# Optimization experiments

Hardware: AMD Instinct MI355X
Metric: run time of the kernel (lower is better)

The kernel has to match this reference:

```python
import jax, jax.numpy as jnp
import numpy as np

N_HEAD = 16

def setup_inputs() -> dict:
    key = jax.random.key(0)
    ks = jax.random.split(key, 9)
    B, S, D = 8, 1024, 1024
    s = 0.02
    return {
        "x":    jax.random.normal(ks[0], (B, S, D), dtype=jnp.float32),
        "mask": jax.random.normal(ks[1], (S, S), dtype=jnp.float32),
        "Wq":   jax.random.normal(ks[2], (D, D), dtype=jnp.float32) * s,
        "bq":   jax.random.normal(ks[3], (D,), dtype=jnp.float32) * s,
        "Wk":   jax.random.normal(ks[4], (D, D), dtype=jnp.float32) * s,
        "Wv":   jax.random.normal(ks[5], (D, D), dtype=jnp.float32) * s,
        "bv":   jax.random.normal(ks[6], (D,), dtype=jnp.float32) * s,
        "Wo":   jax.random.normal(ks[7], (D, D), dtype=jnp.float32) * s,
        "bo":   jax.random.normal(ks[8], (D,), dtype=jnp.float32) * s,
    }

def reference(x, mask, Wq, bq, Wk, Wv, bv, Wo, bo):
    B, S, D = x.shape
    H = N_HEAD
    dh = D // H
    scale = dh ** (-0.25)
    # projections (F.linear: x @ W.T + b); key has no bias
    q = x @ Wq.T + bq
    k = x @ Wk.T
    v = x @ Wv.T + bv
    # [B,S,D] -> [B,H,S,dh]; scale applied to both q and k
    q = q.reshape(B, S, H, dh).transpose(0, 2, 1, 3) * scale
    k = k.reshape(B, S, H, dh).transpose(0, 2, 1, 3) * scale
    v = v.reshape(B, S, H, dh).transpose(0, 2, 1, 3)
    qk = jnp.einsum("bhqd,bhkd->bhqk", q, k) + mask  # [B,H,S,S]
    w = jax.nn.softmax(qk.astype(jnp.float32), axis=-1).astype(q.dtype)
    wv = jnp.einsum("bhqk,bhkd->bhqd", w, v)
    wv = wv.transpose(0, 2, 1, 3).reshape(B, S, D)
    out = wv @ Wo.T + bo
    return out, qk
```

## Files before the change

### kernel.cpp

```cpp
#include <hip/hip_runtime.h>


typedef unsigned short u16;
typedef unsigned int   u32;
typedef __attribute__((ext_vector_type(8)))  __bf16 bf16x8;
typedef __attribute__((ext_vector_type(4)))  float  f32x4;
typedef __attribute__((ext_vector_type(16))) float  f32x16;

__device__ __forceinline__ u16 f2bf(float f) {
  u32 u = __float_as_uint(f);
  u += 0x7FFFu + ((u >> 16) & 1u);
  return (u16)(u >> 16);
}
__device__ __forceinline__ float bf2f(u16 v) {
  return __uint_as_float(((u32)v) << 16);
}
__device__ __forceinline__ u32 pk2(float a, float b) {
  return (u32)f2bf(a) | ((u32)f2bf(b) << 16);
}
__device__ __forceinline__ f32x4 mfma16(bf16x8 a, bf16x8 b, f32x4 c) {
  return __builtin_amdgcn_mfma_f32_16x16x32_bf16(a, b, c, 0, 0, 0);
}
__device__ __forceinline__ f32x16 mfma32(bf16x8 a, bf16x8 b, f32x16 c) {
  return __builtin_amdgcn_mfma_f32_32x32x16_bf16(a, b, c, 0, 0, 0);
}
typedef __attribute__((address_space(3))) u32 lds_u32;
typedef const __attribute__((address_space(1))) u32 glb_u32;
__device__ __forceinline__ void gld_lds16(u16* lds, const u16* g) {
  __builtin_amdgcn_global_load_lds((glb_u32*)g, (lds_u32*)lds, 16, 0, 0);
}
__device__ __forceinline__ bf16x8 ld_bf8(const u16* p) {
  return *(const bf16x8*)p;
}

__global__ __launch_bounds__(256) void cvt_all(
    const float* __restrict__ x,
    const float* __restrict__ Wq, const float* __restrict__ Wk,
    const float* __restrict__ Wv, const float* __restrict__ Wo,
    u16* __restrict__ xb, u16* __restrict__ Wqb, u16* __restrict__ Wkb,
    u16* __restrict__ Wvb, u16* __restrict__ Wob) {
  const size_t i = (size_t)(blockIdx.x * 256 + threadIdx.x) * 8;
  const float* s; u16* d; size_t off;
  if      (i <  8388608) { s = x;  d = xb;  off = i; }
  else if (i <  9437184) { s = Wq; d = Wqb; off = i -  8388608; }
  else if (i < 10485760) { s = Wk; d = Wkb; off = i -  9437184; }
  else if (i < 11534336) { s = Wv; d = Wvb; off = i - 10485760; }
  else                   { s = Wo; d = Wob; off = i - 11534336; }
  const float4* sp = (const float4*)(s + off);
  float4 a = sp[0], b = sp[1];
  u16 r[8];
  r[0] = f2bf(a.x); r[1] = f2bf(a.y); r[2] = f2bf(a.z); r[3] = f2bf(a.w);
  r[4] = f2bf(b.x); r[5] = f2bf(b.y); r[6] = f2bf(b.z); r[7] = f2bf(b.w);
  *(uint4*)(d + off) = *(const uint4*)r;
}

__global__ __launch_bounds__(256) void trans_mask(
    const float* __restrict__ m, u16* __restrict__ mt) {
  __shared__ u16 L[32][33];
  const int x = threadIdx.x & 31, y4 = threadIdx.x >> 5;
  const int r0 = blockIdx.y * 32, c0 = blockIdx.x * 32;
#pragma unroll
  for (int j = 0; j < 4; ++j) {
    const int r = y4 * 4 + j;
    L[x][r] = f2bf(m[(r0 + r) * 1024 + c0 + x]);
  }
  __syncthreads();
#pragma unroll
  for (int j = 0; j < 4; ++j) {
    const int rr = y4 * 4 + j;
    mt[(c0 + rr) * 1024 + r0 + x] = L[rr][x];
  }
}

__global__ __launch_bounds__(256) void mask_pack(
    const u16* __restrict__ mt, u16* __restrict__ mp) {
  const int id = blockIdx.x * 256 + threadIdx.x;
  const int q  = id & 1023;
  const int hi = (id >> 10) & 1;
  const int c  = id >> 11;
  u16 r0[8], r1[8];
#pragma unroll
  for (int r = 0; r < 8; ++r)
    r0[r] = mt[(32 * c + (r & 3) + 8 * (r >> 2) + 4 * hi) * 1024 + q];
#pragma unroll
  for (int r = 8; r < 16; ++r)
    r1[r - 8] = mt[(32 * c + (r & 3) + 8 * (r >> 2) + 4 * hi) * 1024 + q];
  u16* dst = mp + ((size_t)((c * 2 + hi) * 1024 + q)) * 16;
  *(uint4*)dst       = *(const uint4*)r0;
  *(uint4*)(dst + 8) = *(const uint4*)r1;
}

__global__ __launch_bounds__(256) void proj_gemm(
    const u16* __restrict__ xb,
    const u16* __restrict__ Wqb, const u16* __restrict__ Wkb,
    const u16* __restrict__ Wvb,
    const float* __restrict__ bq, const float* __restrict__ bv,
    u16* __restrict__ Qt2, u16* __restrict__ Kt2, u16* __restrict__ V2) {
  __shared__ u16 As[2][128][32];
  __shared__ u16 Bs[2][128][32];
  const int tid  = threadIdx.x;
  const int lane = tid & 63;
  const int wid  = tid >> 6;
  const int c15  = lane & 15, c4 = lane >> 4;
  const int m0   = blockIdx.x * 128;
  const int nv0  = blockIdx.y * 128;
  const int region = nv0 >> 10;
  const int nl0  = nv0 & 1023;
  const u16* Wsrc = (region == 0) ? Wqb : (region == 1) ? Wkb : Wvb;
  const int wrow = wid >> 1, wcol = wid & 1;
  const int srow = lane >> 2, scol = (lane & 3) * 8;

  const u16* aptr = xb   + (m0  + srow) * 1024 + scol;
  const u16* bptr = Wsrc + (nl0 + srow) * 1024 + scol;

  f32x4 acc[4][4] = {};

#pragma unroll
  for (int j = 0; j < 2; ++j) {
    const int r = 64 * j + 16 * wid;
    gld_lds16(&As[0][r][0], aptr + r * 1024);
    gld_lds16(&Bs[0][r][0], bptr + r * 1024);
  }
  __syncthreads();

  int cur = 0;
  for (int k0 = 0; k0 < 1024; k0 += 32) {
    if (k0 + 32 < 1024) {
      const int nxt = cur ^ 1;
#pragma unroll
      for (int j = 0; j < 2; ++j) {
        const int r = 64 * j + 16 * wid;
        gld_lds16(&As[nxt][r][0], aptr + r * 1024 + k0 + 32);
        gld_lds16(&Bs[nxt][r][0], bptr + r * 1024 + k0 + 32);
      }
    }
    bf16x8 af[4], bfr[4];
#pragma unroll
    for (int a = 0; a < 4; ++a) af[a]  = ld_bf8(&As[cur][64 * wrow + 16 * a + c15][8 * c4]);
#pragma unroll
    for (int b = 0; b < 4; ++b) bfr[b] = ld_bf8(&Bs[cur][64 * wcol + 16 * b + c15][8 * c4]);
#pragma unroll
    for (int a = 0; a < 4; ++a)
#pragma unroll
      for (int b = 0; b < 4; ++b)
        acc[a][b] = mfma16(af[a], bfr[b], acc[a][b]);
    __syncthreads();
    cur ^= 1;
  }

  const float kSc = 0.35355339059327373f;
#pragma unroll
  for (int a = 0; a < 4; ++a) {
    const int mg = m0 + 64 * wrow + 16 * a + 4 * c4;
    const int bb = mg >> 10;
    const int sl = mg & 1023;
#pragma unroll
    for (int b = 0; b < 4; ++b) {
      const int nl = 64 * wcol + 16 * b + c15;
      const int nv = nv0 + nl;
      if (region == 0) {
        const int n = nv;
        const float bias = bq[n];
        u16* qp = Qt2 + (((bb * 16 + (n >> 6)) * 8 + ((n >> 3) & 7)) * 1024 + sl) * 8 + (n & 7);
#pragma unroll
        for (int j = 0; j < 4; ++j)
          qp[j * 8] = f2bf((acc[a][b][j] + bias) * kSc);
      } else if (region == 1) {
        const int n = nv - 1024;
        u16* kp = Kt2 + (((bb * 16 + (n >> 6)) * 8 + ((n >> 3) & 7)) * 1024 + sl) * 8 + (n & 7);
#pragma unroll
        for (int j = 0; j < 4; ++j)
          kp[j * 8] = f2bf(acc[a][b][j] * kSc);
      } else {
        const int n = nv - 2048;
        const float bias = bv[n];
        u16* vp = V2 + (((bb * 16 + (n >> 6)) * 128 + (sl >> 3)) * 64 + (n & 63)) * 8 + (sl & 7);
        u16 p[4];
#pragma unroll
        for (int j = 0; j < 4; ++j) p[j] = f2bf(acc[a][b][j] + bias);
        *(uint2*)vp = *(const uint2*)p;
      }
    }
  }
}

__global__ __launch_bounds__(256) void attn_v4(
    const u16* __restrict__ Qt2, const u16* __restrict__ Kt2,
    const u16* __restrict__ V2, const u16* __restrict__ maskP,
    float* __restrict__ qk, u16* __restrict__ WV) {
  __shared__ float Tb[4][32 * 34];
  __shared__ float invl[4][32];
  __shared__ float factw[4][32];
  const int tid  = threadIdx.x;
  const int lane = tid & 63;
  const int w    = tid >> 6;
  const int r31  = lane & 31, hi = lane >> 5;
  const int h = blockIdx.y, b = blockIdx.z;
  const int bh  = b * 16 + h;
  const int q0  = blockIdx.x * 128 + w * 32;
  const int bs0 = b * 1024;

  const u16* qbase = Qt2 + (size_t)bh * 65536;
  const u16* kbase = Kt2 + (size_t)bh * 65536;
  const u16* vbase = V2  + (size_t)bh * 65536;
  float* Tw = Tb[w];
  float* qkbase = qk + ((size_t)bh * 1024 + q0) * 1024;

  bf16x8 qf[4];
#pragma unroll
  for (int kk = 0; kk < 4; ++kk)
    qf[kk] = ld_bf8(qbase + ((2 * kk + hi) * 1024 + q0 + r31) * 8);

  const u16* mrow = maskP + ((size_t)(hi * 1024 + q0 + r31)) * 16;

  float m_run = -3e38f, l = 0.f;
  f32x16 oa0 = {}, oa1 = {};

  bf16x8 kc[4];
#pragma unroll
  for (int kk = 0; kk < 4; ++kk)
    kc[kk] = ld_bf8(kbase + ((2 * kk + hi) * 1024 + r31) * 8);
  bf16x8 mc0 = ld_bf8(mrow);
  bf16x8 mc1 = ld_bf8(mrow + 8);

  for (int c = 0; c < 32; ++c) {
    bf16x8 vf[4];
#pragma unroll
    for (int kk = 0; kk < 2; ++kk) {
      const int sb = 4 * c + 2 * kk + hi;
      vf[2 * kk]     = ld_bf8(vbase + (sb * 64 + r31) * 8);
      vf[2 * kk + 1] = ld_bf8(vbase + (sb * 64 + 32 + r31) * 8);
    }
    const int cn = (c < 31) ? c + 1 : 31;
    bf16x8 kn[4];
#pragma unroll
    for (int kk = 0; kk < 4; ++kk)
      kn[kk] = ld_bf8(kbase + ((2 * kk + hi) * 1024 + 32 * cn + r31) * 8);
    bf16x8 mn0 = ld_bf8(mrow + (size_t)cn * 32768);
    bf16x8 mn1 = ld_bf8(mrow + (size_t)cn * 32768 + 8);

    f32x16 acc = {};
#pragma unroll
    for (int kk = 0; kk < 4; ++kk)
      acc = mfma32(kc[kk], qf[kk], acc);

    float v[16];
    float mloc = -3e38f;
    const u16* mcu0 = (const u16*)&mc0;
    const u16* mcu1 = (const u16*)&mc1;
#pragma unroll
    for (int r = 0; r < 16; ++r) {
      v[r] = acc[r] + bf2f(r < 8 ? mcu0[r] : mcu1[r - 8]);
      mloc = fmaxf(mloc, v[r]);
    }
    mloc = fmaxf(mloc, __shfl_xor(mloc, 32));

#pragma unroll
    for (int g = 0; g < 4; ++g) {
      float2 w0; w0.x = v[4 * g];     w0.y = v[4 * g + 1];
      float2 w1; w1.x = v[4 * g + 2]; w1.y = v[4 * g + 3];
      *(float2*)&Tw[r31 * 34 + 8 * g + 4 * hi]     = w0;
      *(float2*)&Tw[r31 * 34 + 8 * g + 4 * hi + 2] = w1;
    }

    if (!__all(mloc <= m_run + 8.f)) {
      const float m_new = fmaxf(m_run, mloc);
      const float f = __expf(m_run - m_new);
      l *= f;
      if (hi == 0) factw[w][r31] = f;
      asm volatile("s_waitcnt lgkmcnt(0)" ::: "memory");
#pragma unroll
      for (int r = 0; r < 16; ++r) {
        const float fr_ = factw[w][(r & 3) + 8 * (r >> 2) + 4 * hi];
        oa0[r] *= fr_;
        oa1[r] *= fr_;
      }
      m_run = m_new;
    }

#pragma unroll
    for (int qi = 0; qi < 4; ++qi) {
      const int qq = 8 * qi + (lane >> 3);
      const int jj = (lane & 7) * 4;
      float2 u0 = *(const float2*)&Tw[qq * 34 + jj];
      float2 u1 = *(const float2*)&Tw[qq * 34 + jj + 2];
      f32x4 o; o[0] = u0.x; o[1] = u0.y; o[2] = u1.x; o[3] = u1.y;
      *(f32x4*)&qkbase[qq * 1024 + 32 * c + jj] = o;
    }

#pragma unroll
    for (int r = 0; r < 16; ++r) {
      v[r] = __expf(v[r] - m_run);
      l += v[r];
    }

#pragma unroll
    for (int kk = 0; kk < 2; ++kk) {
      const float* pp = v + 8 * kk;
      const u32 a0 = pk2(pp[0], pp[1]), a1 = pk2(pp[2], pp[3]);
      const u32 b0 = pk2(pp[4], pp[5]), b1 = pk2(pp[6], pp[7]);
      const u32 s0 = hi ? a0 : b0, s1 = hi ? a1 : b1;
      const u32 t0 = __shfl_xor(s0, 32), t1 = __shfl_xor(s1, 32);
      union { u32 u[4]; bf16x8 v; } fr;
      fr.u[0] = hi ? t0 : a0;  fr.u[1] = hi ? t1 : a1;
      fr.u[2] = hi ? b0 : t0;  fr.u[3] = hi ? b1 : t1;
      oa0 = mfma32(fr.v, vf[2 * kk],     oa0);
      oa1 = mfma32(fr.v, vf[2 * kk + 1], oa1);
    }

#pragma unroll
    for (int kk = 0; kk < 4; ++kk) kc[kk] = kn[kk];
    mc0 = mn0; mc1 = mn1;
  }

  l += __shfl_xor(l, 32);
  if (hi == 0) invl[w][r31] = 1.0f / l;
  asm volatile("s_waitcnt lgkmcnt(0)" ::: "memory");
#pragma unroll
  for (int r = 0; r < 16; ++r) {
    const int q = (r & 3) + 8 * (r >> 2) + 4 * hi;
    const float iv = invl[w][q];
    u16* wp = WV + (size_t)(bs0 + q0 + q) * 1024 + h * 64;
    wp[r31]      = f2bf(oa0[r] * iv);
    wp[32 + r31] = f2bf(oa1[r] * iv);
  }
}

__global__ __launch_bounds__(256) void out_gemm(
    const u16* __restrict__ Ab, const u16* __restrict__ Wb,
    const float* __restrict__ bias, float* __restrict__ outp) {
  __shared__ u16 As[2][128][32];
  __shared__ u16 Bs[2][128][32];
  const int tid  = threadIdx.x;
  const int lane = tid & 63;
  const int wid  = tid >> 6;
  const int c15  = lane & 15, c4 = lane >> 4;
  const int m0   = blockIdx.x * 128;
  const int n0   = blockIdx.y * 128;
  const int wrow = wid >> 1, wcol = wid & 1;
  const int srow = lane >> 2, scol = (lane & 3) * 8;

  const u16* aptr = Ab + (m0 + srow) * 1024 + scol;
  const u16* bptr = Wb + (n0 + srow) * 1024 + scol;

  f32x4 acc[4][4] = {};

#pragma unroll
  for (int j = 0; j < 2; ++j) {
    const int r = 64 * j + 16 * wid;
    gld_lds16(&As[0][r][0], aptr + r * 1024);
    gld_lds16(&Bs[0][r][0], bptr + r * 1024);
  }
  __syncthreads();

  int cur = 0;
  for (int k0 = 0; k0 < 1024; k0 += 32) {
    if (k0 + 32 < 1024) {
      const int nxt = cur ^ 1;
#pragma unroll
      for (int j = 0; j < 2; ++j) {
        const int r = 64 * j + 16 * wid;
        gld_lds16(&As[nxt][r][0], aptr + r * 1024 + k0 + 32);
        gld_lds16(&Bs[nxt][r][0], bptr + r * 1024 + k0 + 32);
      }
    }
    bf16x8 af[4], bfr[4];
#pragma unroll
    for (int a = 0; a < 4; ++a) af[a]  = ld_bf8(&As[cur][64 * wrow + 16 * a + c15][8 * c4]);
#pragma unroll
    for (int b = 0; b < 4; ++b) bfr[b] = ld_bf8(&Bs[cur][64 * wcol + 16 * b + c15][8 * c4]);
#pragma unroll
    for (int a = 0; a < 4; ++a)
#pragma unroll
      for (int b = 0; b < 4; ++b)
        acc[a][b] = mfma16(af[a], bfr[b], acc[a][b]);
    __syncthreads();
    cur ^= 1;
  }

#pragma unroll
  for (int a = 0; a < 4; ++a) {
    const int mg = m0 + 64 * wrow + 16 * a + 4 * c4;
#pragma unroll
    for (int b = 0; b < 4; ++b) {
      const int ng = n0 + 64 * wcol + 16 * b + c15;
      const float bi = bias[ng];
#pragma unroll
      for (int j = 0; j < 4; ++j)
        outp[(mg + j) * 1024 + ng] = acc[a][b][j] + bi;
    }
  }
}

extern "C" void kernel_launch(void* const* d_in, const int* in_sizes, int n_in,
                              void* d_out, int out_size, void* d_ws, size_t ws_size,
                              hipStream_t stream) {
  const float* x    = (const float*)d_in[0];
  const float* mask = (const float*)d_in[1];
  const float* Wq   = (const float*)d_in[2];
  const float* bq   = (const float*)d_in[3];
  const float* Wk   = (const float*)d_in[4];
  const float* Wv   = (const float*)d_in[5];
  const float* bv   = (const float*)d_in[6];
  const float* Wo   = (const float*)d_in[7];
  const float* bo   = (const float*)d_in[8];

  float* outp = (float*)d_out;
  float* qk   = outp + 8 * 1024 * 1024;

  u16* ws    = (u16*)d_ws;
  u16* xb    = ws;
  u16* Wqb   = xb  + 8388608;
  u16* Wkb   = Wqb + 1048576;
  u16* Wvb   = Wkb + 1048576;
  u16* Wob   = Wvb + 1048576;
  u16* Qt2   = Wob + 1048576;
  u16* Kt2   = Qt2 + 8388608;
  u16* V2    = Kt2 + 8388608;
  u16* WV    = V2  + 8388608;
  u16* maskT = WV  + 8388608;
  u16* maskP = maskT + 1048576;

  cvt_all<<<6144, 256, 0, stream>>>(x, Wq, Wk, Wv, Wo, xb, Wqb, Wkb, Wvb, Wob);
  trans_mask<<<dim3(32, 32), 256, 0, stream>>>(mask, maskT);
  mask_pack<<<256, 256, 0, stream>>>(maskT, maskP);

  proj_gemm<<<dim3(64, 24), 256, 0, stream>>>(xb, Wqb, Wkb, Wvb, bq, bv, Qt2, Kt2, V2);
  attn_v4<<<dim3(8, 16, 8), 256, 0, stream>>>(Qt2, Kt2, V2, maskP, qk, WV);
  out_gemm<<<dim3(64, 8), 256, 0, stream>>>(WV, Wob, bo, outp);
}
```

Before: 319.6 us.

## Replace projection and output GEMMs with 256x256-tile, 4-stage pipelined mainloop

Both the QKV projection and output GEMMs now share a 256x256 tile mainloop run by 512-thread blocks. It uses a 4-deep LDS ring buffer fed by direct global-to-LDS loads, an XOR swizzle against bank conflicts, split A-half MFMA phases with s_setprio, and explicit vmcnt waits. A block-index remap groups tiles for L2 reuse. Larger tiles cut redundant global traffic and improve MFMA-to-load ratio, but the out GEMM now has only 128 blocks, which may underfill the GPU, and each block needs 128KB of LDS.

Result: slower. 349.9 us (+9.5%).

```diff
diff --git a/kernel.cpp b/kernel.cpp
--- a/kernel.cpp
+++ b/kernel.cpp
@@ -90,96 +90,149 @@
   *(uint4*)(dst + 8) = *(const uint4*)r1;
 }
 
-__global__ __launch_bounds__(256) void proj_gemm(
+__device__ __forceinline__ void gemm256_mainloop(
+    const u16* __restrict__ Ag, const u16* __restrict__ Bg,
+    int m0, int n0,
+    u16 (&AS)[4][256][32], u16 (&BS)[4][256][32],
+    f32x4 (&acc)[8][4], int tid) {
+  const int l  = tid & 63, w = tid >> 6;
+  const int c15 = l & 15, c4 = l >> 4;
+  const int wr = w >> 2, wc = w & 3;
+  const int koff = 8 * ((l & 3) ^ ((l >> 2) & 3) ^ ((l >> 4) & 3));
+  const int srow = l >> 2;
+  const int swz = 8 * (c4 ^ (c15 & 3) ^ ((c15 >> 2) & 3));
+  const u16* Abase = Ag + (size_t)(m0 + 32 * w + srow) * 1024 + koff;
+  const u16* Bbase = Bg + (size_t)(n0 + 32 * w + srow) * 1024 + koff;
+
+#define SG_A(slot, g) do { \
+    gld_lds16(&AS[slot][32 * w][0],      Abase + (g) * 32); \
+    gld_lds16(&AS[slot][32 * w + 16][0], Abase + 16384 + (g) * 32); } while (0)
+#define SG_B(slot, g) do { \
+    gld_lds16(&BS[slot][32 * w][0],      Bbase + (g) * 32); \
+    gld_lds16(&BS[slot][32 * w + 16][0], Bbase + 16384 + (g) * 32); } while (0)
+
+  SG_B(0, 0); SG_A(0, 0); SG_B(1, 1); SG_A(1, 1);
+  SG_B(2, 2); SG_A(2, 2); SG_B(3, 3);
+  asm volatile("s_waitcnt vmcnt(10)\n\ts_barrier" ::: "memory");
+
+  for (int h = 0; h < 32; ++h) {
+    const int s = h & 3;
+    SG_A((h + 3) & 3, (h + 3 < 32) ? (h + 3) : 31);
+    bf16x8 bfr[4], afr[4];
+#pragma unroll
+    for (int nf = 0; nf < 4; ++nf)
+      bfr[nf] = ld_bf8(&BS[s][wc * 64 + nf * 16 + c15][0] + swz);
+#pragma unroll
+    for (int mf = 0; mf < 4; ++mf)
+      afr[mf] = ld_bf8(&AS[s][wr * 128 + mf * 16 + c15][0] + swz);
+    __builtin_amdgcn_s_setprio(1);
+#pragma unroll
+    for (int mf = 0; mf < 4; ++mf)
+#pragma unroll
+      for (int nf = 0; nf < 4; ++nf)
+        acc[mf][nf] = mfma16(afr[mf], bfr[nf], acc[mf][nf]);
+    __builtin_amdgcn_s_setprio(0);
+    asm volatile("s_barrier" ::: "memory");
+    SG_B(s, (h + 4 < 32) ? (h + 4) : 31);
+#pragma unroll
+    for (int mf = 0; mf < 4; ++mf)
+      afr[mf] = ld_bf8(&AS[s][wr * 128 + 64 + mf * 16 + c15][0] + swz);
+    __builtin_amdgcn_s_setprio(1);
+#pragma unroll
+    for (int mf = 0; mf < 4; ++mf)
+#pragma unroll
+      for (int nf = 0; nf < 4; ++nf)
+        acc[4 + mf][nf] = mfma16(afr[mf], bfr[nf], acc[4 + mf][nf]);
+    __builtin_amdgcn_s_setprio(0);
+    asm volatile("s_waitcnt vmcnt(10)\n\ts_barrier" ::: "memory");
+  }
+#undef SG_A
+#undef SG_B
+}
+
+__global__ __launch_bounds__(512, 2) void proj256(
     const u16* __restrict__ xb,
     const u16* __restrict__ Wqb, const u16* __restrict__ Wkb,
     const u16* __restrict__ Wvb,
     const float* __restrict__ bq, const float* __restrict__ bv,
     u16* __restrict__ Qt2, u16* __restrict__ Kt2, u16* __restrict__ V2) {
-  __shared__ u16 As[2][128][32];
-  __shared__ u16 Bs[2][128][32];
-  const int tid  = threadIdx.x;
-  const int lane = tid & 63;
-  const int wid  = tid >> 6;
-  const int c15  = lane & 15, c4 = lane >> 4;
-  const int m0   = blockIdx.x * 128;
-  const int nv0  = blockIdx.y * 128;
+  __shared__ u16 AS[4][256][32];
+  __shared__ u16 BS[4][256][32];
+  const int tid = threadIdx.x;
+  const int wg  = blockIdx.x;
+  const int swb = (wg & 7) * 48 + (wg >> 3);
+  const int m0  = (swb & 31) * 256;
+  const int nv0 = (swb >> 5) * 256;
   const int region = nv0 >> 10;
-  const int nl0  = nv0 & 1023;
+  const int nl0 = nv0 & 1023;
   const u16* Wsrc = (region == 0) ? Wqb : (region == 1) ? Wkb : Wvb;
-  const int wrow = wid >> 1, wcol = wid & 1;
-  const int srow = lane >> 2, scol = (lane & 3) * 8;
-
-  const u16* aptr = xb   + (m0  + srow) * 1024 + scol;
-  const u16* bptr = Wsrc + (nl0 + srow) * 1024 + scol;
-
-  f32x4 acc[4][4] = {};
-
-#pragma unroll
-  for (int j = 0; j < 2; ++j) {
-    const int r = 64 * j + 16 * wid;
-    gld_lds16(&As[0][r][0], aptr + r * 1024);
-    gld_lds16(&Bs[0][r][0], bptr + r * 1024);
-  }
-  __syncthreads();
-
-  int cur = 0;
-  for (int k0 = 0; k0 < 1024; k0 += 32) {
-    if (k0 + 32 < 1024) {
-      const int nxt = cur ^ 1;
-#pragma unroll
-      for (int j = 0; j < 2; ++j) {
-        const int r = 64 * j + 16 * wid;
-        gld_lds16(&As[nxt][r][0], aptr + r * 1024 + k0 + 32);
-        gld_lds16(&Bs[nxt][r][0], bptr + r * 1024 + k0 + 32);
-      }
-    }
-    bf16x8 af[4], bfr[4];
-#pragma unroll
-    for (int a = 0; a < 4; ++a) af[a]  = ld_bf8(&As[cur][64 * wrow + 16 * a + c15][8 * c4]);
-#pragma unroll
-    for (int b = 0; b < 4; ++b) bfr[b] = ld_bf8(&Bs[cur][64 * wcol + 16 * b + c15][8 * c4]);
-#pragma unroll
-    for (int a = 0; a < 4; ++a)
-#pragma unroll
-      for (int b = 0; b < 4; ++b)
-        acc[a][b] = mfma16(af[a], bfr[b], acc[a][b]);
-    __syncthreads();
-    cur ^= 1;
-  }
-
+
+  f32x4 acc[8][4] = {};
+  gemm256_mainloop(xb, Wsrc, m0, nl0, AS, BS, acc, tid);
+
+  const int l = tid & 63, w = tid >> 6;
+  const int c15 = l & 15, c4 = l >> 4;
+  const int wr = w >> 2, wc = w & 3;
   const float kSc = 0.35355339059327373f;
 #pragma unroll
-  for (int a = 0; a < 4; ++a) {
-    const int mg = m0 + 64 * wrow + 16 * a + 4 * c4;
+  for (int mf = 0; mf < 8; ++mf) {
+    const int mg = m0 + wr * 128 + mf * 16 + 4 * c4;
     const int bb = mg >> 10;
     const int sl = mg & 1023;
 #pragma unroll
-    for (int b = 0; b < 4; ++b) {
-      const int nl = 64 * wcol + 16 * b + c15;
-      const int nv = nv0 + nl;
+    for (int nf = 0; nf < 4; ++nf) {
+      const int nl = wc * 64 + nf * 16 + c15;
+      const int n  = nl0 + nl;
       if (region == 0) {
-        const int n = nv;
         const float bias = bq[n];
         u16* qp = Qt2 + (((bb * 16 + (n >> 6)) * 8 + ((n >> 3) & 7)) * 1024 + sl) * 8 + (n & 7);
 #pragma unroll
         for (int j = 0; j < 4; ++j)
-          qp[j * 8] = f2bf((acc[a][b][j] + bias) * kSc);
+          qp[j * 8] = f2bf((acc[mf][nf][j] + bias) * kSc);
       } else if (region == 1) {
-        const int n = nv - 1024;
         u16* kp = Kt2 + (((bb * 16 + (n >> 6)) * 8 + ((n >> 3) & 7)) * 1024 + sl) * 8 + (n & 7);
 #pragma unroll
         for (int j = 0; j < 4; ++j)
-          kp[j * 8] = f2bf(acc[a][b][j] * kSc);
+          kp[j * 8] = f2bf(acc[mf][nf][j] * kSc);
       } else {
-        const int n = nv - 2048;
         const float bias = bv[n];
         u16* vp = V2 + (((bb * 16 + (n >> 6)) * 128 + (sl >> 3)) * 64 + (n & 63)) * 8 + (sl & 7);
         u16 p[4];
 #pragma unroll
-        for (int j = 0; j < 4; ++j) p[j] = f2bf(acc[a][b][j] + bias);
+        for (int j = 0; j < 4; ++j) p[j] = f2bf(acc[mf][nf][j] + bias);
         *(uint2*)vp = *(const uint2*)p;
       }
+    }
+  }
+}
+
+__global__ __launch_bounds__(512, 2) void out256(
+    const u16* __restrict__ Ab, const u16* __restrict__ Wb,
+    const float* __restrict__ bias, float* __restrict__ outp) {
+  __shared__ u16 AS[4][256][32];
+  __shared__ u16 BS[4][256][32];
+  const int tid = threadIdx.x;
+  const int wg  = blockIdx.x;
+  const int swb = (wg & 7) * 16 + (wg >> 3);
+  const int m0  = (swb & 31) * 256;
+  const int n0  = (swb >> 5) * 256;
+
+  f32x4 acc[8][4] = {};
+  gemm256_mainloop(Ab, Wb, m0, n0, AS, BS, acc, tid);
+
+  const int l = tid & 63, w = tid >> 6;
+  const int c15 = l & 15, c4 = l >> 4;
+  const int wr = w >> 2, wc = w & 3;
+#pragma unroll
+  for (int mf = 0; mf < 8; ++mf) {
+    const int mg = m0 + wr * 128 + mf * 16 + 4 * c4;
+#pragma unroll
+    for (int nf = 0; nf < 4; ++nf) {
+      const int ng = n0 + wc * 64 + nf * 16 + c15;
+      const float bi = bias[ng];
+#pragma unroll
+      for (int j = 0; j < 4; ++j)
+        outp[(size_t)(mg + j) * 1024 + ng] = acc[mf][nf][j] + bi;
     }
   }
 }
@@ -326,72 +379,6 @@
   }
 }
 
-__global__ __launch_bounds__(256) void out_gemm(
-    const u16* __restrict__ Ab, const u16* __restrict__ Wb,
-    const float* __restrict__ bias, float* __restrict__ outp) {
-  __shared__ u16 As[2][128][32];
-  __shared__ u16 Bs[2][128][32];
-  const int tid  = threadIdx.x;
-  const int lane = tid & 63;
-  const int wid  = tid >> 6;
-  const int c15  = lane & 15, c4 = lane >> 4;
-  const int m0   = blockIdx.x * 128;
-  const int n0   = blockIdx.y * 128;
-  const int wrow = wid >> 1, wcol = wid & 1;
-  const int srow = lane >> 2, scol = (lane & 3) * 8;
-
-  const u16* aptr = Ab + (m0 + srow) * 1024 + scol;
-  const u16* bptr = Wb + (n0 + srow) * 1024 + scol;
-
-  f32x4 acc[4][4] = {};
-
-#pragma unroll
-  for (int j = 0; j < 2; ++j) {
-    const int r = 64 * j + 16 * wid;
-    gld_lds16(&As[0][r][0], aptr + r * 1024);
-    gld_lds16(&Bs[0][r][0], bptr + r * 1024);
-  }
-  __syncthreads();
-
-  int cur = 0;
-  for (int k0 = 0; k0 < 1024; k0 += 32) {
-    if (k0 + 32 < 1024) {
-      const int nxt = cur ^ 1;
-#pragma unroll
-      for (int j = 0; j < 2; ++j) {
-        const int r = 64 * j + 16 * wid;
-        gld_lds16(&As[nxt][r][0], aptr + r * 1024 + k0 + 32);
-        gld_lds16(&Bs[nxt][r][0], bptr + r * 1024 + k0 + 32);
-      }
-    }
-    bf16x8 af[4], bfr[4];
-#pragma unroll
-    for (int a = 0; a < 4; ++a) af[a]  = ld_bf8(&As[cur][64 * wrow + 16 * a + c15][8 * c4]);
-#pragma unroll
-    for (int b = 0; b < 4; ++b) bfr[b] = ld_bf8(&Bs[cur][64 * wcol + 16 * b + c15][8 * c4]);
-#pragma unroll
-    for (int a = 0; a < 4; ++a)
-#pragma unroll
-      for (int b = 0; b < 4; ++b)
-        acc[a][b] = mfma16(af[a], bfr[b], acc[a][b]);
-    __syncthreads();
-    cur ^= 1;
-  }
-
-#pragma unroll
-  for (int a = 0; a < 4; ++a) {
-    const int mg = m0 + 64 * wrow + 16 * a + 4 * c4;
-#pragma unroll
-    for (int b = 0; b < 4; ++b) {
-      const int ng = n0 + 64 * wcol + 16 * b + c15;
-      const float bi = bias[ng];
-#pragma unroll
-      for (int j = 0; j < 4; ++j)
-        outp[(mg + j) * 1024 + ng] = acc[a][b][j] + bi;
-    }
-  }
-}
-
 extern "C" void kernel_launch(void* const* d_in, const int* in_sizes, int n_in,
                               void* d_out, int out_size, void* d_ws, size_t ws_size,
                               hipStream_t stream) {
@@ -425,7 +412,7 @@
   trans_mask<<<dim3(32, 32), 256, 0, stream>>>(mask, maskT);
   mask_pack<<<256, 256, 0, stream>>>(maskT, maskP);
 
-  proj_gemm<<<dim3(64, 24), 256, 0, stream>>>(xb, Wqb, Wkb, Wvb, bq, bv, Qt2, Kt2, V2);
+  proj256<<<384, 512, 0, stream>>>(xb, Wqb, Wkb, Wvb, bq, bv, Qt2, Kt2, V2);
   attn_v4<<<dim3(8, 16, 8), 256, 0, stream>>>(Qt2, Kt2, V2, maskP, qk, WV);
-  out_gemm<<<dim3(64, 8), 256, 0, stream>>>(WV, Wob, bo, outp);
-}
+  out256<<<128, 512, 0, stream>>>(WV, Wob, bo, outp);
+}
```
